# Kernel tuning notes

Measured on AMD Instinct MI355X. Metric: run time of the kernel, lower is better.

The kernel has to match this reference:

```python
import jax, jax.numpy as jnp
import numpy as np

SEQ = 4096
D_IN = 1024
D_QK = 1024
D_V = 1024


def setup_inputs() -> dict:
    key = jax.random.key(0)
    kx, kq, kk, kv = jax.random.split(key, 4)
    x = jax.random.normal(kx, (SEQ, D_IN), dtype=jnp.float32)
    Wq = jax.random.uniform(kq, (D_IN, D_QK), dtype=jnp.float32)
    Wk = jax.random.uniform(kk, (D_IN, D_QK), dtype=jnp.float32)
    Wv = jax.random.uniform(kv, (D_IN, D_V), dtype=jnp.float32)
    return {"x": x, "Wq": Wq, "Wk": Wk, "Wv": Wv}


def reference(x, Wq, Wk, Wv):
    d_qk = Wq.shape[1]
    q = x @ Wq            # [T, d_qk]
    k = x @ Wk            # [T, d_qk]
    v = x @ Wv            # [T, d_v]
    scores = q @ k.T      # [T, T]
    T = scores.shape[0]
    # causal mask: positions j > i are masked with -inf BEFORE scaling
    causal = jnp.tril(jnp.ones((T, T), dtype=bool))
    masked = jnp.where(causal, scores, -jnp.inf)
    attn = jax.nn.softmax(masked / jnp.sqrt(jnp.asarray(d_qk, dtype=scores.dtype)), axis=-1)
    return attn @ v       # [T, d_v]
```

## Files before the change

kernel.cpp:

```cpp
#include <hip/hip_runtime.h>
#include <hip/hip_bf16.h>
#include <stdint.h>
#include <stddef.h>

#define SEQ 4096
#define DIN 1024
#define DQK 1024
#define DV  1024

typedef __bf16 bf16;
typedef __bf16 bf16x4 __attribute__((ext_vector_type(4)));
typedef __bf16 bf16x8 __attribute__((ext_vector_type(8)));
typedef float  f32x4  __attribute__((ext_vector_type(4)));

__global__ __launch_bounds__(256) void split_f32(const float* __restrict__ in,
                                                 bf16* __restrict__ hi,
                                                 bf16* __restrict__ lo, int n4) {
  int i = blockIdx.x * 256 + threadIdx.x;
  if (i >= n4) return;
  const float4 v = ((const float4*)in)[i];
  float a[4] = {v.x, v.y, v.z, v.w};
  bf16x4 h, l;
#pragma unroll
  for (int t = 0; t < 4; ++t) {
    bf16 hh = (bf16)a[t];
    h[t] = hh;
    l[t] = (bf16)(a[t] - (float)hh);
  }
  ((bf16x4*)hi)[i] = h;
  ((bf16x4*)lo)[i] = l;
}

__global__ __launch_bounds__(256) void wtrans_all(
    const float* __restrict__ Wq, const float* __restrict__ Wk,
    const float* __restrict__ Wv, bf16* __restrict__ wqh,
    bf16* __restrict__ wql, bf16* __restrict__ wkh, bf16* __restrict__ wkl,
    bf16* __restrict__ wvt) {
  __shared__ float t[32][33];
  const int g = blockIdx.x >> 10;
  const int bid = blockIdx.x & 1023;
  const float* W = (g == 0) ? Wq : (g == 1) ? Wk : Wv;
  bf16* outH = (g == 0) ? wqh : (g == 1) ? wkh : wvt;
  bf16* outL = (g == 0) ? wql : wkl;
  const bool do_split = (g < 2);
  const int bx = bid & 31;
  const int by = bid >> 5;
  const int tx = threadIdx.x & 31;
  const int ty = threadIdx.x >> 5;
#pragma unroll
  for (int r = 0; r < 32; r += 8)
    t[ty + r][tx] = W[(size_t)(by * 32 + ty + r) * DQK + bx * 32 + tx];
  __syncthreads();
#pragma unroll
  for (int r = 0; r < 32; r += 8) {
    float v = t[tx][ty + r];
    size_t o = (size_t)(bx * 32 + ty + r) * DIN + by * 32 + tx;
    bf16 h = (bf16)v;
    outH[o] = h;
    if (do_split) outL[o] = (bf16)(v - (float)h);
  }
}

__device__ __forceinline__ void stage_tile(const bf16* __restrict__ g, int ld,
                                           int row0, int k0, bf16* lds,
                                           int wid, int lane) {
#pragma unroll
  for (int c = 0; c < 2; ++c) {
    const int q = wid * 2 + c;
    const bf16* src =
        g + (size_t)(row0 + q * 16 + (lane >> 2)) * ld + k0 + (lane & 3) * 8;
    __builtin_amdgcn_global_load_lds(
        (const __attribute__((address_space(1))) void*)src,
        (__attribute__((address_space(3))) void*)(lds + q * 512), 16, 0, 0);
  }
}

__device__ __forceinline__ bf16x8 ldsfrag(const bf16* s, int rbase, int lane) {
  return *(const bf16x8*)&s[(rbase + (lane & 15)) * 32 + ((lane >> 4) * 8)];
}

template <bool SPLIT>
__device__ __forceinline__ void proj_body(
    const bf16* __restrict__ Agh, const bf16* __restrict__ Agl,
    const bf16* __restrict__ Bgh, const bf16* __restrict__ Bgl,
    bf16* __restrict__ outH, bf16* __restrict__ outL, int bm, int bn, int ldo,
    bf16* sAh, bf16* sBh, bf16* sAl, bf16* sBl) {
  const int wid = threadIdx.x >> 6;
  const int lane = threadIdx.x & 63;
  const int wr = (wid >> 1) * 64;
  const int wc = (wid & 1) * 64;

  f32x4 acc[4][4];
#pragma unroll
  for (int i = 0; i < 4; ++i)
#pragma unroll
    for (int j = 0; j < 4; ++j) acc[i][j] = (f32x4)(0.0f);

  for (int kt = 0; kt < DIN / 32; ++kt) {
    const int k0 = kt * 32;
    __syncthreads();
    stage_tile(Agh, DIN, bm * 128, k0, sAh, wid, lane);
    stage_tile(Bgh, DIN, bn * 128, k0, sBh, wid, lane);
    if (SPLIT) {
      stage_tile(Agl, DIN, bm * 128, k0, sAl, wid, lane);
      stage_tile(Bgl, DIN, bn * 128, k0, sBl, wid, lane);
    }
    __syncthreads();

    bf16x8 ah[4], bh[4];
#pragma unroll
    for (int i = 0; i < 4; ++i) ah[i] = ldsfrag(sAh, wr + i * 16, lane);
#pragma unroll
    for (int j = 0; j < 4; ++j) bh[j] = ldsfrag(sBh, wc + j * 16, lane);
#pragma unroll
    for (int i = 0; i < 4; ++i)
#pragma unroll
      for (int j = 0; j < 4; ++j)
        acc[i][j] = __builtin_amdgcn_mfma_f32_16x16x32_bf16(ah[i], bh[j],
                                                            acc[i][j], 0, 0, 0);
    if (SPLIT) {
      bf16x8 bl[4];
#pragma unroll
      for (int j = 0; j < 4; ++j) bl[j] = ldsfrag(sBl, wc + j * 16, lane);
#pragma unroll
      for (int i = 0; i < 4; ++i)
#pragma unroll
        for (int j = 0; j < 4; ++j)
          acc[i][j] = __builtin_amdgcn_mfma_f32_16x16x32_bf16(
              ah[i], bl[j], acc[i][j], 0, 0, 0);
      bf16x8 al[4];
#pragma unroll
      for (int i = 0; i < 4; ++i) al[i] = ldsfrag(sAl, wr + i * 16, lane);
#pragma unroll
      for (int i = 0; i < 4; ++i)
#pragma unroll
        for (int j = 0; j < 4; ++j)
          acc[i][j] = __builtin_amdgcn_mfma_f32_16x16x32_bf16(
              al[i], bh[j], acc[i][j], 0, 0, 0);
    }
  }

  const int r0 = bm * 128 + wr + ((lane >> 4) * 4);
  const int c0 = bn * 128 + wc + (lane & 15);
#pragma unroll
  for (int i = 0; i < 4; ++i)
#pragma unroll
    for (int j = 0; j < 4; ++j)
#pragma unroll
      for (int r = 0; r < 4; ++r) {
        const size_t o = (size_t)(r0 + i * 16 + r) * ldo + (c0 + j * 16);
        const float v = acc[i][j][r];
        bf16 h = (bf16)v;
        outH[o] = h;
        if (SPLIT) outL[o] = (bf16)(v - (float)h);
      }
}

__global__ __launch_bounds__(256, 2) void fused_proj(
    const bf16* __restrict__ xh, const bf16* __restrict__ xl,
    const bf16* __restrict__ wqh, const bf16* __restrict__ wql,
    const bf16* __restrict__ wkh, const bf16* __restrict__ wkl,
    const bf16* __restrict__ wvt, bf16* __restrict__ qh, bf16* __restrict__ ql,
    bf16* __restrict__ kh, bf16* __restrict__ kl, bf16* __restrict__ vt) {
  __shared__ bf16 sAh[128 * 32];
  __shared__ bf16 sBh[128 * 32];
  __shared__ bf16 sAl[128 * 32];
  __shared__ bf16 sBl[128 * 32];
  const int b = blockIdx.x;
  if (b < 256) {
    proj_body<true>(xh, xl, wqh, wql, qh, ql, b >> 3, b & 7, DQK, sAh, sBh, sAl,
                    sBl);
  } else if (b < 512) {
    const int bb = b - 256;
    proj_body<true>(xh, xl, wkh, wkl, kh, kl, bb >> 3, bb & 7, DQK, sAh, sBh,
                    sAl, sBl);
  } else {
    const int bb = b - 512;
    proj_body<false>(wvt, nullptr, xh, nullptr, vt, nullptr, bb >> 5, bb & 31,
                     SEQ, sAh, sBh, sAl, sBl);
  }
}

__global__ __launch_bounds__(256, 2) void score1(const bf16* __restrict__ qh,
                                                 const bf16* __restrict__ kh,
                                                 float* __restrict__ S) {
  __shared__ bf16 sA[128 * 32];
  __shared__ bf16 sB[128 * 32];
  const int t = blockIdx.x;
  int bi = (int)((sqrtf(8.0f * (float)t + 1.0f) - 1.0f) * 0.5f);
  while ((bi + 1) * (bi + 2) / 2 <= t) ++bi;
  while (bi * (bi + 1) / 2 > t) --bi;
  const int bm = bi;
  const int bn = t - bi * (bi + 1) / 2;

  const int wid = threadIdx.x >> 6;
  const int lane = threadIdx.x & 63;
  const int wr = (wid >> 1) * 64;
  const int wc = (wid & 1) * 64;

  f32x4 acc[4][4];
#pragma unroll
  for (int i = 0; i < 4; ++i)
#pragma unroll
    for (int j = 0; j < 4; ++j) acc[i][j] = (f32x4)(0.0f);

  for (int kt = 0; kt < DQK / 32; ++kt) {
    const int k0 = kt * 32;
    __syncthreads();
    stage_tile(qh, DQK, bm * 128, k0, sA, wid, lane);
    stage_tile(kh, DQK, bn * 128, k0, sB, wid, lane);
    __syncthreads();
    bf16x8 a[4], b[4];
#pragma unroll
    for (int i = 0; i < 4; ++i) a[i] = ldsfrag(sA, wr + i * 16, lane);
#pragma unroll
    for (int j = 0; j < 4; ++j) b[j] = ldsfrag(sB, wc + j * 16, lane);
#pragma unroll
    for (int i = 0; i < 4; ++i)
#pragma unroll
      for (int j = 0; j < 4; ++j)
        acc[i][j] = __builtin_amdgcn_mfma_f32_16x16x32_bf16(a[i], b[j],
                                                            acc[i][j], 0, 0, 0);
  }

  const int r0 = bm * 128 + wr + ((lane >> 4) * 4);
  const int c0 = bn * 128 + wc + (lane & 15);
#pragma unroll
  for (int i = 0; i < 4; ++i)
#pragma unroll
    for (int j = 0; j < 4; ++j)
#pragma unroll
      for (int r = 0; r < 4; ++r)
        S[(size_t)(r0 + i * 16 + r) * SEQ + (c0 + j * 16)] = acc[i][j][r];
}

__global__ __launch_bounds__(256) void softmax_fixup(
    float* __restrict__ S, const bf16* __restrict__ qh,
    const bf16* __restrict__ ql, const bf16* __restrict__ kh,
    const bf16* __restrict__ kl) {
  __shared__ __align__(16) float rb[4][4096];
  const int wid = threadIdx.x >> 6;
  const int lane = threadIdx.x & 63;
  const int row = blockIdx.x * 4 + wid;
  const int len = row + 1;
  const int ext = ((row >> 7) + 1) << 7;
  float* srow = S + (size_t)row * SEQ;
  float* rbw = rb[wid];

  float m0 = -3.0e38f;
  for (int j = lane * 4; j < len; j += 256) {
    float4 v = *(const float4*)(srow + j);
    *(float4*)&rbw[j] = v;
    if (j + 0 < len) m0 = fmaxf(m0, v.x);
    if (j + 1 < len) m0 = fmaxf(m0, v.y);
    if (j + 2 < len) m0 = fmaxf(m0, v.z);
    if (j + 3 < len) m0 = fmaxf(m0, v.w);
  }
#pragma unroll
  for (int o = 32; o > 0; o >>= 1) m0 = fmaxf(m0, __shfl_xor(m0, o));
  __syncthreads();

  float q[16];
  {
    const size_t base = (size_t)row * DQK + lane * 16;
    bf16x8 h0 = *(const bf16x8*)(qh + base);
    bf16x8 h1 = *(const bf16x8*)(qh + base + 8);
    bf16x8 l0 = *(const bf16x8*)(ql + base);
    bf16x8 l1 = *(const bf16x8*)(ql + base + 8);
#pragma unroll
    for (int t = 0; t < 8; ++t) {
      q[t] = (float)h0[t] + (float)l0[t];
      q[8 + t] = (float)h1[t] + (float)l1[t];
    }
  }

  const float T = m0 - 1024.0f;
  float m = -3.0e38f;
  for (int base = 0; base < len; base += 64) {
    const int j = base + lane;
    const bool cand = (j < len) && (rbw[j] >= T);
    unsigned long long mask = __ballot(cand);
    while (mask) {
      const int jj = base + (int)__builtin_ctzll(mask);
      mask &= mask - 1;
      const size_t kb = (size_t)jj * DQK + lane * 16;
      bf16x8 h0 = *(const bf16x8*)(kh + kb);
      bf16x8 h1 = *(const bf16x8*)(kh + kb + 8);
      bf16x8 l0 = *(const bf16x8*)(kl + kb);
      bf16x8 l1 = *(const bf16x8*)(kl + kb + 8);
      float d = 0.f;
#pragma unroll
      for (int t = 0; t < 8; ++t) {
        d += q[t] * ((float)h0[t] + (float)l0[t]);
        d += q[8 + t] * ((float)h1[t] + (float)l1[t]);
      }
#pragma unroll
      for (int o = 32; o > 0; o >>= 1) d += __shfl_xor(d, o);
      if (lane == 0) rbw[jj] = d;
      m = fmaxf(m, d);
    }
  }
  __syncthreads();

  float lsum = 0.f;
  for (int j = lane * 4; j < len; j += 256) {
    float4 v = *(float4*)&rbw[j];
    float4 e;
    e.x = (j + 0 < len) ? __expf((v.x - m) * 0.03125f) : 0.f;
    e.y = (j + 1 < len) ? __expf((v.y - m) * 0.03125f) : 0.f;
    e.z = (j + 2 < len) ? __expf((v.z - m) * 0.03125f) : 0.f;
    e.w = (j + 3 < len) ? __expf((v.w - m) * 0.03125f) : 0.f;
    *(float4*)&rbw[j] = e;
    lsum += e.x + e.y + e.z + e.w;
  }
#pragma unroll
  for (int o = 32; o > 0; o >>= 1) lsum += __shfl_xor(lsum, o);
  const float inv = 1.0f / lsum;
  __syncthreads();

  bf16* prow = (bf16*)srow;
  for (int j = lane * 8; j < ext; j += 512) {
    bf16x8 o8;
#pragma unroll
    for (int t = 0; t < 8; ++t) {
      const int jj = j + t;
      const float v = (jj < len) ? rbw[jj] * inv : 0.f;
      o8[t] = (bf16)v;
    }
    *(bf16x8*)(prow + j) = o8;
  }
}

__global__ __launch_bounds__(256, 2) void pv_kernel(const bf16* __restrict__ P,
                                                    const bf16* __restrict__ vt,
                                                    float* __restrict__ out,
                                                    float* __restrict__ part) {
  __shared__ bf16 sA[128 * 32];
  __shared__ bf16 sB[128 * 32];
  const int g = blockIdx.x >> 3;
  const int bn = blockIdx.x & 7;
  int bm, slice;
  if (g < 8) {
    bm = g;
    slice = 0;
  } else if (g < 24) {
    const int i = g - 8;
    bm = 8 + (i >> 1);
    slice = i & 1;
  } else if (g < 48) {
    const int i = g - 24;
    bm = 16 + i / 3;
    slice = i % 3;
  } else {
    const int i = g - 48;
    bm = 24 + (i >> 2);
    slice = i & 3;
  }
  const int ks0 = slice * 32;
  const int kend = (bm + 1) * 4;
  const int nk = (ks0 + 32 < kend) ? ks0 + 32 : kend;

  const int wid = threadIdx.x >> 6;
  const int lane = threadIdx.x & 63;
  const int wr = (wid >> 1) * 64;
  const int wc = (wid & 1) * 64;

  f32x4 acc[4][4];
#pragma unroll
  for (int i = 0; i < 4; ++i)
#pragma unroll
    for (int j = 0; j < 4; ++j) acc[i][j] = (f32x4)(0.0f);

  for (int kt = ks0; kt < nk; ++kt) {
    const int k0 = kt * 32;
    __syncthreads();
    stage_tile(P, 2 * SEQ, bm * 128, k0, sA, wid, lane);
    stage_tile(vt, SEQ, bn * 128, k0, sB, wid, lane);
    __syncthreads();
    bf16x8 a[4], b[4];
#pragma unroll
    for (int i = 0; i < 4; ++i) a[i] = ldsfrag(sA, wr + i * 16, lane);
#pragma unroll
    for (int j = 0; j < 4; ++j) b[j] = ldsfrag(sB, wc + j * 16, lane);
#pragma unroll
    for (int i = 0; i < 4; ++i)
#pragma unroll
      for (int j = 0; j < 4; ++j)
        acc[i][j] = __builtin_amdgcn_mfma_f32_16x16x32_bf16(a[i], b[j],
                                                            acc[i][j], 0, 0, 0);
  }

  float* dst;
  int rbase;
  if (slice == 0) {
    dst = out;
    rbase = 0;
  } else if (slice == 1) {
    dst = part;
    rbase = 1024;
  } else if (slice == 2) {
    dst = part + 3145728;
    rbase = 2048;
  } else {
    dst = part + 5242880;
    rbase = 3072;
  }
  const int r0 = bm * 128 + wr + ((lane >> 4) * 4);
  const int c0 = bn * 128 + wc + (lane & 15);
#pragma unroll
  for (int i = 0; i < 4; ++i)
#pragma unroll
    for (int j = 0; j < 4; ++j)
#pragma unroll
      for (int r = 0; r < 4; ++r)
        dst[(size_t)(r0 + i * 16 + r - rbase) * DV + (c0 + j * 16)] =
            acc[i][j][r];
}

__global__ __launch_bounds__(256) void pv_reduce(const float* __restrict__ part,
                                                 float* __restrict__ out) {
  const int idx = blockIdx.x * 256 + threadIdx.x;
  const int r = 1024 + (idx >> 8);
  const int c4 = (idx & 255) * 4;
  const size_t o = (size_t)r * DV + c4;
  float4 acc = *(float4*)&out[o];
  const float4 p1 = *(const float4*)&part[(size_t)(r - 1024) * DV + c4];
  acc.x += p1.x; acc.y += p1.y; acc.z += p1.z; acc.w += p1.w;
  if (r >= 2048) {
    const float4 p2 =
        *(const float4*)&part[3145728 + (size_t)(r - 2048) * DV + c4];
    acc.x += p2.x; acc.y += p2.y; acc.z += p2.z; acc.w += p2.w;
  }
  if (r >= 3072) {
    const float4 p3 =
        *(const float4*)&part[5242880 + (size_t)(r - 3072) * DV + c4];
    acc.x += p3.x; acc.y += p3.y; acc.z += p3.z; acc.w += p3.w;
  }
  *(float4*)&out[o] = acc;
}

extern "C" void kernel_launch(void* const* d_in, const int* in_sizes, int n_in,
                              void* d_out, int out_size, void* d_ws,
                              size_t ws_size, hipStream_t stream) {
  const float* x = (const float*)d_in[0];
  const float* Wq = (const float*)d_in[1];
  const float* Wk = (const float*)d_in[2];
  const float* Wv = (const float*)d_in[3];
  float* out = (float*)d_out;
  char* ws = (char*)d_ws;

  const size_t MB = 1024 * 1024;
  const size_t OFF_QH = 0, OFF_QL = 8 * MB, OFF_KH = 16 * MB, OFF_KL = 24 * MB;
  const size_t OFF_PART = 0;
  const size_t OFF_VT = 32 * MB;
  const size_t OFF_S = 40 * MB;
  const size_t OFF_XH = 40 * MB, OFF_XL = 48 * MB;
  const size_t OFF_WQH = 56 * MB, OFF_WQL = 58 * MB;
  const size_t OFF_WKH = 60 * MB, OFF_WKL = 62 * MB, OFF_WVT = 64 * MB;
  const size_t NEEDED = 104 * MB;
  if (ws_size < NEEDED) return;

  bf16* qh = (bf16*)(ws + OFF_QH);
  bf16* ql = (bf16*)(ws + OFF_QL);
  bf16* kh = (bf16*)(ws + OFF_KH);
  bf16* kl = (bf16*)(ws + OFF_KL);
  float* part = (float*)(ws + OFF_PART);
  bf16* vt = (bf16*)(ws + OFF_VT);
  float* S = (float*)(ws + OFF_S);
  bf16* xh = (bf16*)(ws + OFF_XH);
  bf16* xl = (bf16*)(ws + OFF_XL);
  bf16* wqh = (bf16*)(ws + OFF_WQH);
  bf16* wql = (bf16*)(ws + OFF_WQL);
  bf16* wkh = (bf16*)(ws + OFF_WKH);
  bf16* wkl = (bf16*)(ws + OFF_WKL);
  bf16* wvt = (bf16*)(ws + OFF_WVT);

  split_f32<<<(SEQ * DIN / 4 + 255) / 256, 256, 0, stream>>>(x, xh, xl,
                                                             SEQ * DIN / 4);
  wtrans_all<<<3072, 256, 0, stream>>>(Wq, Wk, Wv, wqh, wql, wkh, wkl, wvt);

  fused_proj<<<768, 256, 0, stream>>>(xh, xl, wqh, wql, wkh, wkl, wvt, qh, ql,
                                      kh, kl, vt);

  score1<<<(SEQ / 128) * (SEQ / 128 + 1) / 2, 256, 0, stream>>>(qh, kh, S);

  softmax_fixup<<<SEQ / 4, 256, 0, stream>>>(S, qh, ql, kh, kl);

  pv_kernel<<<640, 256, 0, stream>>>((const bf16*)S, vt, out, part);

  pv_reduce<<<(SEQ - 1024) * DV / 4 / 256, 256, 0, stream>>>(part, out);
}
```

Measured before the change: 185.8 us.

## Drop per-row LDS buffer in softmax fixup; batch candidate dot products per wave

The softmax fixup kernel no longer stages each whole score row in a 16KB LDS buffer. It rereads the scores from global memory, builds a compacted candidate list with LDS atomics, and computes exact fp32 dot products for eight candidates at a time, each split across eight lanes. It then recomputes the exponentials when it writes bf16 probabilities in place. The much smaller LDS footprint should allow more resident blocks, and the parallel candidate processing cuts serialized wave reductions. The cost is extra global rereads and repeated exp work, plus a hard cap of 256 candidates per row that silently drops any extras.

```diff
diff --git a/kernel.cpp b/kernel.cpp
--- a/kernel.cpp
+++ b/kernel.cpp
@@ -238,96 +238,117 @@
     float* __restrict__ S, const bf16* __restrict__ qh,
     const bf16* __restrict__ ql, const bf16* __restrict__ kh,
     const bf16* __restrict__ kl) {
-  __shared__ __align__(16) float rb[4][4096];
+  __shared__ __align__(16) float qf[4][1024];
+  __shared__ int lists[4][256];
+  __shared__ int cnts[4];
   const int wid = threadIdx.x >> 6;
   const int lane = threadIdx.x & 63;
   const int row = blockIdx.x * 4 + wid;
   const int len = row + 1;
   const int ext = ((row >> 7) + 1) << 7;
   float* srow = S + (size_t)row * SEQ;
-  float* rbw = rb[wid];
-
-  float m0 = -3.0e38f;
-  for (int j = lane * 4; j < len; j += 256) {
-    float4 v = *(const float4*)(srow + j);
-    *(float4*)&rbw[j] = v;
-    if (j + 0 < len) m0 = fmaxf(m0, v.x);
-    if (j + 1 < len) m0 = fmaxf(m0, v.y);
-    if (j + 2 < len) m0 = fmaxf(m0, v.z);
-    if (j + 3 < len) m0 = fmaxf(m0, v.w);
-  }
-#pragma unroll
-  for (int o = 32; o > 0; o >>= 1) m0 = fmaxf(m0, __shfl_xor(m0, o));
-  __syncthreads();
-
-  float q[16];
+
+  if (lane == 0) cnts[wid] = 0;
   {
     const size_t base = (size_t)row * DQK + lane * 16;
     bf16x8 h0 = *(const bf16x8*)(qh + base);
     bf16x8 h1 = *(const bf16x8*)(qh + base + 8);
     bf16x8 l0 = *(const bf16x8*)(ql + base);
     bf16x8 l1 = *(const bf16x8*)(ql + base + 8);
+    float* dst = &qf[wid][lane * 16];
 #pragma unroll
     for (int t = 0; t < 8; ++t) {
-      q[t] = (float)h0[t] + (float)l0[t];
-      q[8 + t] = (float)h1[t] + (float)l1[t];
-    }
-  }
+      dst[t] = (float)h0[t] + (float)l0[t];
+      dst[8 + t] = (float)h1[t] + (float)l1[t];
+    }
+  }
+  __syncthreads();
+
+  float m0 = -3.0e38f;
+  for (int j = lane * 4; j < len; j += 256) {
+    float4 v = *(const float4*)(srow + j);
+    if (j + 0 < len) m0 = fmaxf(m0, v.x);
+    if (j + 1 < len) m0 = fmaxf(m0, v.y);
+    if (j + 2 < len) m0 = fmaxf(m0, v.z);
+    if (j + 3 < len) m0 = fmaxf(m0, v.w);
+  }
+#pragma unroll
+  for (int o = 32; o > 0; o >>= 1) m0 = fmaxf(m0, __shfl_xor(m0, o));
 
   const float T = m0 - 1024.0f;
+  for (int j = lane * 4; j < len; j += 256) {
+    float4 v = *(const float4*)(srow + j);
+    float va[4] = {v.x, v.y, v.z, v.w};
+#pragma unroll
+    for (int t = 0; t < 4; ++t) {
+      if (j + t < len && va[t] >= T) {
+        int p = atomicAdd(&cnts[wid], 1);
+        if (p < 256) lists[wid][p] = j + t;
+      }
+    }
+  }
+  int cnt = cnts[wid];
+  if (cnt > 256) cnt = 256;
+
+  const int cslot = lane >> 3;
+  const int seg = lane & 7;
+  const float* qfr = qf[wid];
   float m = -3.0e38f;
-  for (int base = 0; base < len; base += 64) {
-    const int j = base + lane;
-    const bool cand = (j < len) && (rbw[j] >= T);
-    unsigned long long mask = __ballot(cand);
-    while (mask) {
-      const int jj = base + (int)__builtin_ctzll(mask);
-      mask &= mask - 1;
-      const size_t kb = (size_t)jj * DQK + lane * 16;
-      bf16x8 h0 = *(const bf16x8*)(kh + kb);
-      bf16x8 h1 = *(const bf16x8*)(kh + kb + 8);
-      bf16x8 l0 = *(const bf16x8*)(kl + kb);
-      bf16x8 l1 = *(const bf16x8*)(kl + kb + 8);
-      float d = 0.f;
-#pragma unroll
-      for (int t = 0; t < 8; ++t) {
-        d += q[t] * ((float)h0[t] + (float)l0[t]);
-        d += q[8 + t] * ((float)h1[t] + (float)l1[t]);
+  for (int b = 0; b < cnt; b += 8) {
+    const int idx = b + cslot;
+    const bool valid = idx < cnt;
+    const int jj = valid ? lists[wid][idx] : 0;
+    float d = valid ? 0.f : -3.0e38f;
+    if (valid) {
+      const bf16* khr = kh + (size_t)jj * DQK;
+      const bf16* klr = kl + (size_t)jj * DQK;
+#pragma unroll 4
+      for (int g = 0; g < 16; ++g) {
+        const int e0 = g * 64 + seg * 8;
+        bf16x8 h = *(const bf16x8*)(khr + e0);
+        bf16x8 l = *(const bf16x8*)(klr + e0);
+#pragma unroll
+        for (int t = 0; t < 8; ++t)
+          d += qfr[e0 + t] * ((float)h[t] + (float)l[t]);
       }
-#pragma unroll
-      for (int o = 32; o > 0; o >>= 1) d += __shfl_xor(d, o);
-      if (lane == 0) rbw[jj] = d;
-      m = fmaxf(m, d);
-    }
-  }
-  __syncthreads();
+    }
+#pragma unroll
+    for (int o = 1; o < 8; o <<= 1) {
+      float od = __shfl_xor(d, o);
+      d = valid ? d + od : d;
+    }
+    if (valid && seg == 0) srow[jj] = d;
+    m = fmaxf(m, d);
+  }
+#pragma unroll
+  for (int o = 32; o > 0; o >>= 1) m = fmaxf(m, __shfl_xor(m, o));
+
+  __threadfence();
 
   float lsum = 0.f;
   for (int j = lane * 4; j < len; j += 256) {
-    float4 v = *(float4*)&rbw[j];
-    float4 e;
-    e.x = (j + 0 < len) ? __expf((v.x - m) * 0.03125f) : 0.f;
-    e.y = (j + 1 < len) ? __expf((v.y - m) * 0.03125f) : 0.f;
-    e.z = (j + 2 < len) ? __expf((v.z - m) * 0.03125f) : 0.f;
-    e.w = (j + 3 < len) ? __expf((v.w - m) * 0.03125f) : 0.f;
-    *(float4*)&rbw[j] = e;
-    lsum += e.x + e.y + e.z + e.w;
+    float4 v = *(const float4*)(srow + j);
+    lsum += (j + 0 < len) ? __expf((v.x - m) * 0.03125f) : 0.f;
+    lsum += (j + 1 < len) ? __expf((v.y - m) * 0.03125f) : 0.f;
+    lsum += (j + 2 < len) ? __expf((v.z - m) * 0.03125f) : 0.f;
+    lsum += (j + 3 < len) ? __expf((v.w - m) * 0.03125f) : 0.f;
   }
 #pragma unroll
   for (int o = 32; o > 0; o >>= 1) lsum += __shfl_xor(lsum, o);
   const float inv = 1.0f / lsum;
-  __syncthreads();
 
   bf16* prow = (bf16*)srow;
-  for (int j = lane * 8; j < ext; j += 512) {
-    bf16x8 o8;
-#pragma unroll
-    for (int t = 0; t < 8; ++t) {
-      const int jj = j + t;
-      const float v = (jj < len) ? rbw[jj] * inv : 0.f;
-      o8[t] = (bf16)v;
-    }
-    *(bf16x8*)(prow + j) = o8;
+  for (int j = lane * 4; j < ext; j += 256) {
+    float4 v = *(const float4*)(srow + j);
+    float va[4] = {v.x, v.y, v.z, v.w};
+    bf16x4 o4;
+#pragma unroll
+    for (int t = 0; t < 4; ++t) {
+      const float e =
+          (j + t < len) ? __expf((va[t] - m) * 0.03125f) * inv : 0.f;
+      o4[t] = (bf16)e;
+    }
+    *(bf16x4*)(prow + j) = o4;
   }
 }
 
```

After: 289.7 us. +55.9%, slower.
